# Kernel optimization log

Hardware: AMD Instinct MI355X
Metric: run time of the kernel (lower is better)

The kernel has to match this reference:

```python
import jax, jax.numpy as jnp
import numpy as np

N = 100000      # nodes
E = 1600000     # edges
F_IN = 256      # nfeat
F_OUT = 128     # out channels


def setup_inputs() -> dict:
    key = jax.random.key(0)
    k1, k2, k3 = jax.random.split(key, 3)
    feature = jax.random.normal(k1, (N, F_IN), dtype=jnp.float32)
    edge_index = jax.random.randint(k2, (2, E), 0, N, dtype=jnp.int32)
    # glorot-ish init for the GCN linear weight
    W = jax.random.normal(k3, (F_IN, F_OUT), dtype=jnp.float32) * (1.0 / np.sqrt(F_IN))
    b = jnp.zeros((F_OUT,), dtype=jnp.float32)
    return {"feature": feature, "edge_index": edge_index, "W": W, "b": b}


def reference(feature, edge_index, W, b):
    # GCNConv (PyG defaults): add self-loops, symmetric normalization,
    # linear transform then scatter-add aggregation to destination nodes.
    x = feature @ W                                   # [N, F_OUT]
    loops = jnp.arange(N, dtype=edge_index.dtype)
    row = jnp.concatenate([edge_index[0], loops])     # source nodes [E+N]
    col = jnp.concatenate([edge_index[1], loops])     # dest   nodes [E+N]
    ones = jnp.ones(row.shape[0], dtype=x.dtype)
    deg = jax.ops.segment_sum(ones, col, num_segments=N)   # in-degree incl. self-loop
    dinv = jnp.where(deg > 0, jax.lax.rsqrt(deg), 0.0)     # deg^{-1/2}
    norm = dinv[row] * dinv[col]                            # [E+N]
    msg = x[row] * norm[:, None]                            # gather + scale
    agg = jax.ops.segment_sum(msg, col, num_segments=N)     # scatter-add
    x_out = jax.nn.relu(agg + b)                            # [N, F_OUT]
    h = jax.nn.sigmoid(jnp.mean(x_out, axis=0))             # [F_OUT]
    return (x_out, h)
```

## Files before the change

### kernel.cpp

```cpp
#include <hip/hip_runtime.h>
#include <hip/hip_bf16.h>

typedef __attribute__((ext_vector_type(8))) short short8;
typedef __attribute__((ext_vector_type(4))) float floatx4;
typedef unsigned short u16;
typedef unsigned int u32;

#define F_IN  256
#define F_OUT 128
#define CAP   64
#define CA    24
#define CB    40
#define NWIN  8
#define PRE   24

__device__ __forceinline__ float bf_lo(u32 u) { return __uint_as_float(u << 16); }
__device__ __forceinline__ float bf_hi(u32 u) { return __uint_as_float(u & 0xffff0000u); }
__device__ __forceinline__ u16 f2bf(float f) {
    u32 u = __float_as_uint(f);
    u += 0x7fffu + ((u >> 16) & 1u);
    return (u16)(u >> 16);
}

__global__ void k_pack(const float* __restrict__ W, u16* __restrict__ Wp,
                       u16* __restrict__ xw, int N) {
    int gid = blockIdx.x * 256 + threadIdx.x;
    if (gid < 32768) {
        int f = gid >> 3, j = gid & 7;
        int lane = f & 63, tt = (f >> 6) & 7, kb = f >> 9;
        int m = lane & 15, q = lane >> 4;
        Wp[(size_t)f * 8 + j] = f2bf(W[(kb * 32 + q * 8 + j) * F_OUT + tt * 16 + m]);
    } else {
        int e = gid - 32768;
        if (e < 128) {
            int w = e >> 4, m = e & 15;
            xw[((size_t)w * (N + 1) + N) * 16 + m] = 0;
        }
    }
}

__global__ void k_fillcap_xcd(const int* __restrict__ rowi, const int* __restrict__ coli,
                              int E, int npw, int N,
                              int* __restrict__ cursor,
                              int* __restrict__ csrA, int* __restrict__ csrB) {
    int grp  = blockIdx.x & (NWIN - 1);
    int gblk = blockIdx.x >> 3;
    int nblk = gridDim.x >> 3;
    int lo = grp * npw;
    int hi = lo + npw; if (hi > N) hi = N;
    const int stride = nblk * blockDim.x;
    int e = gblk * blockDim.x + threadIdx.x;
    for (; e + stride < E; e += 2 * stride) {
        int d0 = coli[e],          r0 = rowi[e];
        int d1 = coli[e + stride], r1 = rowi[e + stride];
        if (d0 >= lo && d0 < hi) {
            int p = atomicAdd(&cursor[d0], 1);
            if (p < CA) csrA[d0 * CA + p] = r0;
            else if (p < CAP) csrB[d0 * CB + (p - CA)] = r0;
        }
        if (d1 >= lo && d1 < hi) {
            int p = atomicAdd(&cursor[d1], 1);
            if (p < CA) csrA[d1 * CA + p] = r1;
            else if (p < CAP) csrB[d1 * CB + (p - CA)] = r1;
        }
    }
    if (e < E) {
        int d = coli[e], r = rowi[e];
        if (d >= lo && d < hi) {
            int p = atomicAdd(&cursor[d], 1);
            if (p < CA) csrA[d * CA + p] = r;
            else if (p < CAP) csrB[d * CB + (p - CA)] = r;
        }
    }
}

__global__ void k_degree(const int* __restrict__ col, int E, int* __restrict__ deg) {
    for (int e = blockIdx.x * blockDim.x + threadIdx.x; e < E; e += gridDim.x * blockDim.x)
        atomicAdd(&deg[col[e]], 1);
}

__global__ void k_blocksum(const int* __restrict__ deg, int N, int* __restrict__ bsum) {
    __shared__ int s[256];
    int base = blockIdx.x * 1024, t = threadIdx.x;
    int v = 0;
    for (int i = t; i < 1024; i += 256) { int idx = base + i; v += (idx < N) ? deg[idx] : 0; }
    s[t] = v; __syncthreads();
    for (int off = 128; off > 0; off >>= 1) {
        if (t < off) s[t] += s[t + off];
        __syncthreads();
    }
    if (t == 0) bsum[blockIdx.x] = s[0];
}

__global__ void k_rowptr(const int* __restrict__ deg, int N, const int* __restrict__ bsum,
                         int nb, int* __restrict__ rowptr) {
    __shared__ int s[256];
    __shared__ int sb[256];
    int base = blockIdx.x * 1024, t = threadIdx.x;
    sb[t] = (t < nb && t < blockIdx.x) ? bsum[t] : 0;
    __syncthreads();
    for (int off = 128; off > 0; off >>= 1) {
        if (t < off) sb[t] += sb[t + off];
        __syncthreads();
    }
    int blockbase = sb[0];
    int v[4]; int tot = 0;
#pragma unroll
    for (int j = 0; j < 4; ++j) {
        int idx = base + t * 4 + j;
        v[j] = (idx < N) ? deg[idx] : 0;
        tot += v[j];
    }
    s[t] = tot; __syncthreads();
    for (int off = 1; off < 256; off <<= 1) {
        int x = (t >= off) ? s[t - off] : 0;
        __syncthreads();
        s[t] += x;
        __syncthreads();
    }
    int prefix = blockbase + s[t] - tot;
#pragma unroll
    for (int j = 0; j < 4; ++j) {
        int idx = base + t * 4 + j;
        if (idx < N) rowptr[idx] = prefix;
        prefix += v[j];
    }
}

__global__ void k_fill(const int* __restrict__ rowi, const int* __restrict__ coli, int E,
                       const int* __restrict__ rowptr, int* __restrict__ cursor,
                       int* __restrict__ csr) {
    for (int e = blockIdx.x * blockDim.x + threadIdx.x; e < E; e += gridDim.x * blockDim.x) {
        int d = coli[e];
        int p = atomicAdd(&cursor[d], 1);
        csr[rowptr[d] + p] = rowi[e];
    }
}

__global__ __launch_bounds__(256) void k_gemm(
        const float* __restrict__ feat, const int* __restrict__ deg,
        const u16* __restrict__ Wp, u16* __restrict__ xw, int N) {
    __shared__ u16 atile[64 * 264];
    const int t = threadIdx.x, wave = t >> 6, lane = t & 63;
    const int m = lane & 15, q = lane >> 4;
    const int base = blockIdx.x * 64;

    for (int r = wave; r < 64; r += 4) {
        int i = base + r;
        float ax = 0.f, ay = 0.f, az = 0.f, aw = 0.f;
        if (i < N) {
            float di = rsqrtf((float)(deg[i] + 1));
            float4 v = *(const float4*)(feat + (size_t)i * F_IN + lane * 4);
            ax = di * v.x; ay = di * v.y; az = di * v.z; aw = di * v.w;
        }
        u32* dst = (u32*)(atile + r * 264 + lane * 4);
        dst[0] = ((u32)f2bf(ay) << 16) | (u32)f2bf(ax);
        dst[1] = ((u32)f2bf(aw) << 16) | (u32)f2bf(az);
    }
    __syncthreads();

    floatx4 acc[8];
#pragma unroll
    for (int tt = 0; tt < 8; ++tt) acc[tt] = (floatx4)0.0f;
    const short8* wp = (const short8*)Wp;
#pragma unroll
    for (int kb = 0; kb < 8; ++kb) {
        short8 a0 = *(const short8*)(atile + (wave * 16 + m) * 264 + kb * 32 + q * 8);
#pragma unroll
        for (int tt = 0; tt < 8; ++tt) {
            short8 b = wp[(kb * 8 + tt) * 64 + lane];
            acc[tt] = __builtin_amdgcn_mfma_f32_16x16x32_bf16(a0, b, acc[tt], 0, 0, 0);
        }
    }

#pragma unroll
    for (int r = 0; r < 4; ++r) {
        int orow = base + wave * 16 + q * 4 + r;
        if (orow < N) {
#pragma unroll
            for (int tt = 0; tt < 8; ++tt)
                xw[((size_t)tt * (N + 1) + orow) * 16 + m] = f2bf(acc[tt][r]);
        }
    }
}

__global__ __launch_bounds__(256) void k_agg(const u16* __restrict__ xw,
                                             const int* __restrict__ rowptr,
                                             const int* __restrict__ deg,
                                             const int* __restrict__ csr,
                                             const int* __restrict__ csrB,
                                             const float* __restrict__ bvec,
                                             float* __restrict__ out,
                                             float* __restrict__ hsum, int N) {
    __shared__ float hpart[16];
    int t = threadIdx.x;
    if (t < 16) hpart[t] = 0.f;
    __syncthreads();
    const int w = blockIdx.x & 7;
    const int stripe = blockIdx.x >> 3;
    const int nstripe = gridDim.x >> 3;
    const int lane = t & 63, wv = t >> 6;
    const int lane7 = lane & 7;
    const int g = lane >> 3;
    const int gbase = lane & 56;
    const u32* slice = (const u32*)xw + (size_t)w * (N + 1) * 8;
    float b0 = bvec[w * 16 + 2 * lane7], b1 = bvec[w * 16 + 2 * lane7 + 1];
    float h0 = 0.f, h1 = 0.f;
    const int step = nstripe * 32;

    int i = stripe * 32 + wv * 8 + g;
    int dd_c = 0, s0_c = 0, sA_c = N, sB_c = N, sC_c = N;
    if (i < N) {
        dd_c = deg[i];
        s0_c = rowptr ? rowptr[i] : i * CA;
        sA_c = csr[s0_c + lane7];
        sB_c = csr[s0_c + 8 + lane7];
        sC_c = csr[s0_c + 16 + lane7];
    }
    while (i < N) {
        int inext = i + step;
        int dd_n = 0, s0_n = 0, sA_n = N, sB_n = N, sC_n = N;
        if (inext < N) {
            dd_n = deg[inext];
            s0_n = rowptr ? rowptr[inext] : inext * CA;
            sA_n = csr[s0_n + lane7];
            sB_n = csr[s0_n + 8 + lane7];
            sC_n = csr[s0_n + 16 + lane7];
        }
        int dd = dd_c;
        float di = rsqrtf((float)(dd + 1));
        if (!rowptr) dd = dd < CAP ? dd : CAP;
        u32 xs = slice[(u32)(i * 8 + lane7)];
        float a0 = bf_lo(xs), a1 = bf_hi(xs);
        int sA = (lane7 < dd)      ? sA_c : N;
        int sB = (lane7 + 8 < dd)  ? sB_c : N;
        int sC = (lane7 + 16 < dd) ? sC_c : N;
        u32 xv[PRE];
#pragma unroll
        for (int u = 0; u < 8; ++u) {
            int sx = __shfl(sA, gbase + u);
            xv[u] = slice[(u32)(sx * 8 + lane7)];
        }
#pragma unroll
        for (int u = 0; u < 8; ++u) {
            int sx = __shfl(sB, gbase + u);
            xv[8 + u] = slice[(u32)(sx * 8 + lane7)];
        }
#pragma unroll
        for (int u = 0; u < 8; ++u) {
            int sx = __shfl(sC, gbase + u);
            xv[16 + u] = slice[(u32)(sx * 8 + lane7)];
        }
#pragma unroll
        for (int u = 0; u < PRE; ++u) { a0 += bf_lo(xv[u]); a1 += bf_hi(xv[u]); }
        if (__any(dd > PRE)) {
            int ddmax = dd;
            ddmax = max(ddmax, __shfl_xor(ddmax, 8));
            ddmax = max(ddmax, __shfl_xor(ddmax, 16));
            ddmax = max(ddmax, __shfl_xor(ddmax, 32));
            ddmax = min(ddmax, rowptr ? (1 << 20) : CAP);
            int s0 = s0_c;
            for (int jb = PRE; jb < ddmax; jb += 8) {
                int sxv = N;
                if (jb + lane7 < dd) {
                    if (rowptr) sxv = csr[s0 + jb + lane7];
                    else        sxv = csrB[i * CB + (jb - CA) + lane7];
                }
                u32 yv[8];
#pragma unroll
                for (int u = 0; u < 8; ++u) {
                    int sx = __shfl(sxv, gbase + u);
                    yv[u] = slice[(u32)(sx * 8 + lane7)];
                }
#pragma unroll
                for (int u = 0; u < 8; ++u) { a0 += bf_lo(yv[u]); a1 += bf_hi(yv[u]); }
            }
        }
        float o0 = fmaxf(fmaf(a0, di, b0), 0.f);
        float o1 = fmaxf(fmaf(a1, di, b1), 0.f);
        h0 += o0; h1 += o1;
        *(float2*)(out + (size_t)i * F_OUT + w * 16 + 2 * lane7) = make_float2(o0, o1);
        i = inext;
        dd_c = dd_n; s0_c = s0_n; sA_c = sA_n; sB_c = sB_n; sC_c = sC_n;
    }
    atomicAdd(&hpart[2 * lane7], h0);
    atomicAdd(&hpart[2 * lane7 + 1], h1);
    __syncthreads();
    if (t < 16) atomicAdd(&hsum[w * 16 + t], hpart[t]);
}

__global__ void k_h(const float* __restrict__ hsum, float* __restrict__ outh, float invN) {
    int t = threadIdx.x;
    if (t < 128) {
        float mm = hsum[t] * invN;
        outh[t] = 1.f / (1.f + __expf(-mm));
    }
}

extern "C" void kernel_launch(void* const* d_in, const int* in_sizes, int n_in,
                              void* d_out, int out_size, void* d_ws, size_t ws_size,
                              hipStream_t stream) {
    const float* feat = (const float*)d_in[0];
    const int* ei     = (const int*)d_in[1];
    const float* W    = (const float*)d_in[2];
    const float* bvec = (const float*)d_in[3];
    float* out        = (float*)d_out;

    const int N = in_sizes[0] / F_IN;
    const int E = in_sizes[1] / 2;

    char* ws = (char*)d_ws;
    size_t o = 0;
    u16* Wp       = (u16*)(ws + o);   o += (size_t)F_IN * F_OUT * 2;
    int* deg      = (int*)(ws + o);   o += (size_t)N * 4;
    int* cursor   = (int*)(ws + o);   o += (size_t)N * 4;
    float* hsum   = (float*)(ws + o); o += 512;
    int* rowptr   = (int*)(ws + o);   o += (size_t)N * 4;
    int* bsum     = (int*)(ws + o);   o += 1024;
    size_t fixed  = o;

    size_t xw_bytes = (size_t)(N + 1) * F_OUT * 2;
    size_t need_fast = fixed + (size_t)N * (CA + CB) * 4 + xw_bytes;
    bool fast = ws_size >= need_fast + 4096;
    int npw = (N + NWIN - 1) / NWIN;

    if (fast) {
        int* csrA = (int*)(ws + o);   o += (size_t)N * CA * 4;
        int* csrB = (int*)(ws + o);   o += (size_t)N * CB * 4;
        u16* xw   = (u16*)(ws + o);   o += xw_bytes;

        hipMemsetAsync((char*)cursor, 0, (size_t)N * 4 + 512, stream);
        k_pack<<<129, 256, 0, stream>>>(W, Wp, xw, N);
        k_fillcap_xcd<<<2048, 256, 0, stream>>>(ei, ei + E, E, npw, N, cursor,
                                                csrA, csrB);
        int ntiles = (N + 63) / 64;
        k_gemm<<<ntiles, 256, 0, stream>>>(feat, cursor, Wp, xw, N);
        k_agg<<<2048, 256, 0, stream>>>(xw, nullptr, cursor, csrA, csrB,
                                        bvec, out, hsum, N);
        k_h<<<1, 128, 0, stream>>>(hsum, out + (size_t)N * F_OUT, 1.0f / (float)N);
    } else {
        int* csr = (int*)(ws + o);    o += (size_t)E * 4;
        u16* xw  = (u16*)(ws + o);    o += xw_bytes;

        hipMemsetAsync((char*)deg, 0, (size_t)N * 8 + 512, stream);
        k_pack<<<129, 256, 0, stream>>>(W, Wp, xw, N);
        k_degree<<<1024, 256, 0, stream>>>(ei + E, E, deg);
        int nb = (N + 1023) / 1024;
        k_blocksum<<<nb, 256, 0, stream>>>(deg, N, bsum);
        k_rowptr<<<nb, 256, 0, stream>>>(deg, N, bsum, nb, rowptr);
        k_fill<<<1024, 256, 0, stream>>>(ei, ei + E, E, rowptr, cursor, csr);
        int ntiles = (N + 63) / 64;
        k_gemm<<<ntiles, 256, 0, stream>>>(feat, deg, Wp, xw, N);
        k_agg<<<2048, 256, 0, stream>>>(xw, rowptr, deg, csr, nullptr,
                                        bvec, out, hsum, N);
        k_h<<<1, 128, 0, stream>>>(hsum, out + (size_t)N * F_OUT, 1.0f / (float)N);
    }
}
```

Before: 348.3 us.

## Fold memset into pack kernel, fuse sigmoid into agg tail, double fill grid

Removes the separate hipMemsetAsync by zeroing the cursor, hsum and done counter inside k_pack. Drops the k_h launch by having the last finishing k_agg block, detected with an atomic counter, compute the sigmoid of the mean. Doubles the k_fillcap_xcd grid and switches the bf16 packing and accumulation to packed intrinsics and vector types. The aim is fewer launches and cheaper per-element math, at the cost of a threadfence and atomic counter at the end of k_agg.

Result: slower. 412.5 us (+18.4%).

```diff
diff --git a/kernel.cpp b/kernel.cpp
--- a/kernel.cpp
+++ b/kernel.cpp
@@ -3,6 +3,7 @@
 
 typedef __attribute__((ext_vector_type(8))) short short8;
 typedef __attribute__((ext_vector_type(4))) float floatx4;
+typedef __attribute__((ext_vector_type(2))) float f32x2;
 typedef unsigned short u16;
 typedef unsigned int u32;
 
@@ -23,19 +24,21 @@
 }
 
 __global__ void k_pack(const float* __restrict__ W, u16* __restrict__ Wp,
-                       u16* __restrict__ xw, int N) {
+                       u16* __restrict__ xw, int* __restrict__ zero0,
+                       int nzero, int N) {
     int gid = blockIdx.x * 256 + threadIdx.x;
     if (gid < 32768) {
         int f = gid >> 3, j = gid & 7;
         int lane = f & 63, tt = (f >> 6) & 7, kb = f >> 9;
         int m = lane & 15, q = lane >> 4;
         Wp[(size_t)f * 8 + j] = f2bf(W[(kb * 32 + q * 8 + j) * F_OUT + tt * 16 + m]);
+    } else if (gid < 32896) {
+        int e = gid - 32768;
+        int w = e >> 4, m = e & 15;
+        xw[((size_t)w * (N + 1) + N) * 16 + m] = 0;
     } else {
-        int e = gid - 32768;
-        if (e < 128) {
-            int w = e >> 4, m = e & 15;
-            xw[((size_t)w * (N + 1) + N) * 16 + m] = 0;
-        }
+        int z = gid - 32896;
+        if (z < nzero) zero0[z] = 0;
     }
 }
 
@@ -153,9 +156,11 @@
             float4 v = *(const float4*)(feat + (size_t)i * F_IN + lane * 4);
             ax = di * v.x; ay = di * v.y; az = di * v.z; aw = di * v.w;
         }
+        __hip_bfloat162 p0 = __float22bfloat162_rn(float2{ax, ay});
+        __hip_bfloat162 p1 = __float22bfloat162_rn(float2{az, aw});
         u32* dst = (u32*)(atile + r * 264 + lane * 4);
-        dst[0] = ((u32)f2bf(ay) << 16) | (u32)f2bf(ax);
-        dst[1] = ((u32)f2bf(aw) << 16) | (u32)f2bf(az);
+        dst[0] = *(u32*)&p0;
+        dst[1] = *(u32*)&p1;
     }
     __syncthreads();
 
@@ -191,8 +196,12 @@
                                              const int* __restrict__ csrB,
                                              const float* __restrict__ bvec,
                                              float* __restrict__ out,
-                                             float* __restrict__ hsum, int N) {
+                                             float* __restrict__ hsum,
+                                             int* __restrict__ done,
+                                             float* __restrict__ outh,
+                                             float invN, int N) {
     __shared__ float hpart[16];
+    __shared__ int lastflag;
     int t = threadIdx.x;
     if (t < 16) hpart[t] = 0.f;
     __syncthreads();
@@ -205,7 +214,7 @@
     const int gbase = lane & 56;
     const u32* slice = (const u32*)xw + (size_t)w * (N + 1) * 8;
     float b0 = bvec[w * 16 + 2 * lane7], b1 = bvec[w * 16 + 2 * lane7 + 1];
-    float h0 = 0.f, h1 = 0.f;
+    f32x2 h = (f32x2)0.f;
     const int step = nstripe * 32;
 
     int i = stripe * 32 + wv * 8 + g;
@@ -231,7 +240,7 @@
         float di = rsqrtf((float)(dd + 1));
         if (!rowptr) dd = dd < CAP ? dd : CAP;
         u32 xs = slice[(u32)(i * 8 + lane7)];
-        float a0 = bf_lo(xs), a1 = bf_hi(xs);
+        f32x2 a; a.x = bf_lo(xs); a.y = bf_hi(xs);
         int sA = (lane7 < dd)      ? sA_c : N;
         int sB = (lane7 + 8 < dd)  ? sB_c : N;
         int sC = (lane7 + 16 < dd) ? sC_c : N;
@@ -252,7 +261,10 @@
             xv[16 + u] = slice[(u32)(sx * 8 + lane7)];
         }
 #pragma unroll
-        for (int u = 0; u < PRE; ++u) { a0 += bf_lo(xv[u]); a1 += bf_hi(xv[u]); }
+        for (int u = 0; u < PRE; ++u) {
+            f32x2 tv; tv.x = bf_lo(xv[u]); tv.y = bf_hi(xv[u]);
+            a += tv;
+        }
         if (__any(dd > PRE)) {
             int ddmax = dd;
             ddmax = max(ddmax, __shfl_xor(ddmax, 8));
@@ -273,27 +285,36 @@
                     yv[u] = slice[(u32)(sx * 8 + lane7)];
                 }
 #pragma unroll
-                for (int u = 0; u < 8; ++u) { a0 += bf_lo(yv[u]); a1 += bf_hi(yv[u]); }
+                for (int u = 0; u < 8; ++u) {
+                    f32x2 tv; tv.x = bf_lo(yv[u]); tv.y = bf_hi(yv[u]);
+                    a += tv;
+                }
             }
         }
-        float o0 = fmaxf(fmaf(a0, di, b0), 0.f);
-        float o1 = fmaxf(fmaf(a1, di, b1), 0.f);
-        h0 += o0; h1 += o1;
+        float o0 = fmaxf(fmaf(a.x, di, b0), 0.f);
+        float o1 = fmaxf(fmaf(a.y, di, b1), 0.f);
+        h.x += o0; h.y += o1;
         *(float2*)(out + (size_t)i * F_OUT + w * 16 + 2 * lane7) = make_float2(o0, o1);
         i = inext;
         dd_c = dd_n; s0_c = s0_n; sA_c = sA_n; sB_c = sB_n; sC_c = sC_n;
     }
-    atomicAdd(&hpart[2 * lane7], h0);
-    atomicAdd(&hpart[2 * lane7 + 1], h1);
+    atomicAdd(&hpart[2 * lane7], h.x);
+    atomicAdd(&hpart[2 * lane7 + 1], h.y);
     __syncthreads();
     if (t < 16) atomicAdd(&hsum[w * 16 + t], hpart[t]);
-}
-
-__global__ void k_h(const float* __restrict__ hsum, float* __restrict__ outh, float invN) {
-    int t = threadIdx.x;
-    if (t < 128) {
-        float mm = hsum[t] * invN;
-        outh[t] = 1.f / (1.f + __expf(-mm));
+    __syncthreads();
+    if (t == 0) {
+        __threadfence();
+        int old = atomicAdd(done, 1);
+        lastflag = (old == (int)gridDim.x - 1);
+    }
+    __syncthreads();
+    if (lastflag) {
+        __threadfence();
+        if (t < 128) {
+            float mm = atomicAdd(&hsum[t], 0.f) * invN;
+            outh[t] = 1.f / (1.f + __expf(-mm));
+        }
     }
 }
 
@@ -315,6 +336,7 @@
     int* deg      = (int*)(ws + o);   o += (size_t)N * 4;
     int* cursor   = (int*)(ws + o);   o += (size_t)N * 4;
     float* hsum   = (float*)(ws + o); o += 512;
+    int* done     = (int*)(ws + o);   o += 64;
     int* rowptr   = (int*)(ws + o);   o += (size_t)N * 4;
     int* bsum     = (int*)(ws + o);   o += 1024;
     size_t fixed  = o;
@@ -323,27 +345,29 @@
     size_t need_fast = fixed + (size_t)N * (CA + CB) * 4 + xw_bytes;
     bool fast = ws_size >= need_fast + 4096;
     int npw = (N + NWIN - 1) / NWIN;
+    float invN = 1.0f / (float)N;
+    float* outh = out + (size_t)N * F_OUT;
 
     if (fast) {
         int* csrA = (int*)(ws + o);   o += (size_t)N * CA * 4;
         int* csrB = (int*)(ws + o);   o += (size_t)N * CB * 4;
         u16* xw   = (u16*)(ws + o);   o += xw_bytes;
 
-        hipMemsetAsync((char*)cursor, 0, (size_t)N * 4 + 512, stream);
-        k_pack<<<129, 256, 0, stream>>>(W, Wp, xw, N);
-        k_fillcap_xcd<<<2048, 256, 0, stream>>>(ei, ei + E, E, npw, N, cursor,
+        int nzero = N + 144;
+        int packblocks = (32896 + nzero + 255) / 256;
+        k_pack<<<packblocks, 256, 0, stream>>>(W, Wp, xw, cursor, nzero, N);
+        k_fillcap_xcd<<<4096, 256, 0, stream>>>(ei, ei + E, E, npw, N, cursor,
                                                 csrA, csrB);
         int ntiles = (N + 63) / 64;
         k_gemm<<<ntiles, 256, 0, stream>>>(feat, cursor, Wp, xw, N);
         k_agg<<<2048, 256, 0, stream>>>(xw, nullptr, cursor, csrA, csrB,
-                                        bvec, out, hsum, N);
-        k_h<<<1, 128, 0, stream>>>(hsum, out + (size_t)N * F_OUT, 1.0f / (float)N);
+                                        bvec, out, hsum, done, outh, invN, N);
     } else {
         int* csr = (int*)(ws + o);    o += (size_t)E * 4;
         u16* xw  = (u16*)(ws + o);    o += xw_bytes;
 
-        hipMemsetAsync((char*)deg, 0, (size_t)N * 8 + 512, stream);
-        k_pack<<<129, 256, 0, stream>>>(W, Wp, xw, N);
+        hipMemsetAsync((char*)deg, 0, (size_t)N * 8 + 576, stream);
+        k_pack<<<129, 256, 0, stream>>>(W, Wp, xw, cursor, 0, N);
         k_degree<<<1024, 256, 0, stream>>>(ei + E, E, deg);
         int nb = (N + 1023) / 1024;
         k_blocksum<<<nb, 256, 0, stream>>>(deg, N, bsum);
@@ -352,7 +376,6 @@
         int ntiles = (N + 63) / 64;
         k_gemm<<<ntiles, 256, 0, stream>>>(feat, deg, Wp, xw, N);
         k_agg<<<2048, 256, 0, stream>>>(xw, rowptr, deg, csr, nullptr,
-                                        bvec, out, hsum, N);
-        k_h<<<1, 128, 0, stream>>>(hsum, out + (size_t)N * F_OUT, 1.0f / (float)N);
-    }
-}
+                                        bvec, out, hsum, done, outh, invN, N);
+    }
+}
```
